# Performance work log

Hardware: AMD Instinct MI355X
Metric: run time of the kernel (lower is better)

## Reference

```python
import jax, jax.numpy as jnp
import numpy as np

B, T, S1, S2 = 8, 64, 128, 128
TD, SD, V, PAD = 512, 512, 32000, 0
EXT = V + S1 + S2
EPS = 1e-5


def _ln(x):
    # F.layer_norm with no affine params (biased variance, eps=1e-5)
    m = x.mean(axis=-1, keepdims=True)
    v = ((x - m) ** 2).mean(axis=-1, keepdims=True)
    return (x - m) / jnp.sqrt(v + EPS)


def _cross_attention(q, k, q_mask, k_mask, attn_w, attn_b, v_vec):
    # attn(cat(q,k)) == q @ Wq^T + k @ Wk^T + b, computed without materializing the concat
    Wq = attn_w[:, :TD]          # [TD, TD] (query part of weight: cat order is (query, key))
    Wk = attn_w[:, TD:]          # [TD, SD]
    sq = jnp.einsum('btd,ed->bte', q, Wq)   # [B,T,TD]
    sk = jnp.einsum('bsd,ed->bse', k, Wk)   # [B,S,TD]
    energy = jnp.tanh(sq[:, :, None, :] + sk[:, None, :, :] + attn_b)  # [B,T,S,TD]
    scores = jnp.einsum('btse,e->bts', energy, v_vec)                  # [B,T,S]
    out_att = scores * k_mask[:, None, :] * q_mask[:, :, None]
    masked = jnp.where((k_mask == PAD)[:, None, :], -jnp.inf, scores)
    attn = jax.nn.softmax(masked, axis=-1)
    weight = jnp.einsum('bts,bsd->btd', attn, k) * q_mask[:, :, None]  # [B,T,SD]
    return out_att, weight


def _scatter_copy(att, map_idx):
    # index_put_(accumulate=True) into [B,T,EXT]
    copy = jnp.zeros((B, T, EXT), dtype=att.dtype)
    b_idx = jnp.arange(B)[:, None, None]
    t_idx = jnp.arange(T)[None, :, None]
    m_idx = map_idx[:, None, :]
    return copy.at[b_idx, t_idx, m_idx].add(att)


def setup_inputs() -> dict:
    key = jax.random.key(0)
    ks = jax.random.split(key, 14)
    sc = 0.02
    return {
        'tgt_dec_out': jax.random.normal(ks[0], (B, T, TD), jnp.float32),
        'src1_key': jax.random.normal(ks[1], (B, S1, SD), jnp.float32),
        'src2_key': jax.random.normal(ks[2], (B, S2, SD), jnp.float32),
        'src1_map_idx': jax.random.randint(ks[3], (B, S1), 0, EXT),
        'src2_map_idx': jax.random.randint(ks[4], (B, S2), 0, EXT),
        'out_fc_w': jax.random.normal(ks[5], (V, TD), jnp.float32) * sc,
        'out_fc_b': jnp.zeros((V,), jnp.float32),
        'attn1_w': jax.random.normal(ks[6], (TD, SD + TD), jnp.float32) * sc,
        'attn1_b': jnp.zeros((TD,), jnp.float32),
        'v1': jax.random.normal(ks[7], (TD,), jnp.float32) * sc,
        'attn2_w': jax.random.normal(ks[8], (TD, SD + TD), jnp.float32) * sc,
        'attn2_b': jnp.zeros((TD,), jnp.float32),
        'v2': jax.random.normal(ks[9], (TD,), jnp.float32) * sc,
        'gate_w': jax.random.normal(ks[10], (3, 2 * SD + TD), jnp.float32) * sc,
        'gate_b': jnp.zeros((3,), jnp.float32),
    }


def reference(tgt_dec_out, src1_key, src2_key, src1_map_idx, src2_map_idx,
              out_fc_w, out_fc_b, attn1_w, attn1_b, v1, attn2_w, attn2_b, v2,
              gate_w, gate_b):
    tgt_output = _ln(jnp.einsum('btd,vd->btv', tgt_dec_out, out_fc_w) + out_fc_b)
    tgt_output = jnp.pad(tgt_output, ((0, 0), (0, 0), (0, S1 + S2)), constant_values=float(PAD))

    tgt_mask = jnp.sign(jnp.abs(tgt_dec_out).sum(-1))   # [B,T]
    src1_mask = jnp.sign(jnp.abs(src1_key).sum(-1))     # [B,S1]
    src2_mask = jnp.sign(jnp.abs(src2_key).sum(-1))     # [B,S2]

    att1, c1 = _cross_attention(tgt_dec_out, src1_key, tgt_mask, src1_mask, attn1_w, attn1_b, v1)
    att1 = _ln(att1)
    copy_output1 = _scatter_copy(att1, src1_map_idx)

    att2, c2 = _cross_attention(tgt_dec_out, src2_key, tgt_mask, src2_mask, attn2_w, attn2_b, v2)
    att2 = _ln(att2)
    copy_output2 = _scatter_copy(att2, src2_map_idx)

    gate_in = jnp.concatenate([tgt_dec_out, c1, c2], axis=-1)  # [B,T,TD+2*SD]
    p = jax.nn.softmax(jnp.einsum('btd,pd->btp', gate_in, gate_w) + gate_b, axis=-1)  # [B,T,3]

    output = (tgt_output * p[..., 0:1]
              + copy_output1 * p[..., 1:2]
              + copy_output2 * p[..., 2:3])
    return output
```

## Files before the change

kernel.cpp:

```cpp
#include <hip/hip_runtime.h>

#define NB 8
#define NT 64
#define NS 128
#define TDIM 512
#define NV 32000
#define NEXT 32256
#define NBT 512
#define LNEPS 1e-5f
#define CLG 2.8853900817779268f

typedef unsigned short u16;
typedef __attribute__((ext_vector_type(8))) short short8;
typedef __attribute__((ext_vector_type(4))) float f32x4;

__device__ __forceinline__ float bf2f(u16 u){ union{unsigned int i; float f;} v; v.i = ((unsigned int)u)<<16; return v.f; }
__device__ __forceinline__ u16 f2bf(float f){ union{float f; unsigned int i;} v; v.f=f; unsigned int r = v.i + 0x7FFFu + ((v.i>>16)&1u); return (u16)(r>>16); }
__device__ __forceinline__ float wsum(float v){
  v += __shfl_xor(v,32); v += __shfl_xor(v,16); v += __shfl_xor(v,8);
  v += __shfl_xor(v,4);  v += __shfl_xor(v,2);  v += __shfl_xor(v,1); return v; }
__device__ __forceinline__ float wmax(float v){
  v = fmaxf(v,__shfl_xor(v,32)); v = fmaxf(v,__shfl_xor(v,16)); v = fmaxf(v,__shfl_xor(v,8));
  v = fmaxf(v,__shfl_xor(v,4));  v = fmaxf(v,__shfl_xor(v,2));  v = fmaxf(v,__shfl_xor(v,1)); return v; }

#define GL2LDS(gp, lp) __builtin_amdgcn_global_load_lds( \
    (__attribute__((address_space(1))) void*)(void*)(gp), \
    (__attribute__((address_space(3))) void*)(void*)(lp), 16, 0, 0)

__global__ __launch_bounds__(256) void k_cast(const float* tgt, const float* s1, const float* s2,
    const float* a1w, const float* a2w, const float* ofw,
    u16* tgtb, u16* s1b, u16* s2b, u16* a1wb, u16* a2wb, u16* ofwb, float* msk)
{
  int blk = blockIdx.x;
  const float* src; u16* dst; int base;
  if(blk < 128){       src=tgt; dst=tgtb;  base=blk; }
  else if(blk < 384){  src=s1;  dst=s1b;   base=blk-128; }
  else if(blk < 640){  src=s2;  dst=s2b;   base=blk-384; }
  else if(blk < 896){  src=a1w; dst=a1wb;  base=blk-640; }
  else if(blk < 1152){ src=a2w; dst=a2wb;  base=blk-896; }
  else {               src=ofw; dst=ofwb;  base=blk-1152; }
  size_t off = (size_t)base*2048 + (size_t)threadIdx.x*8;
  float4 x0 = *(const float4*)(src+off);
  float4 x1 = *(const float4*)(src+off+4);
  float xs[8] = {x0.x,x0.y,x0.z,x0.w,x1.x,x1.y,x1.z,x1.w};
  short8 r;
  #pragma unroll
  for(int j=0;j<8;++j) r[j] = (short)f2bf(xs[j]);
  *(short8*)(dst+off) = r;
  if(blk < 640){
    float a = 0.f;
    #pragma unroll
    for(int j=0;j<8;++j) a += fabsf(xs[j]);
    a = wsum(a);
    if((threadIdx.x&63)==0){
      int w = threadIdx.x>>6;
      int midx;
      if(blk<128)      midx = blk*4 + w;
      else if(blk<384) midx = 512 + (blk-128)*4 + w;
      else             midx = 1536 + (blk-384)*4 + w;
      msk[midx] = (a>0.f) ? 1.f : 0.f;
    }
  }
}

template<int MODE>
__device__ __forceinline__ void gemm_core(const u16* A, int lda, const u16* W, int ldw,
    float* Cf, u16* Cb, int ldc, const float* bias, int K, int bm, int bn, float scale,
    float2* pstats, int nb)
{
  __shared__ u16 Al[128*32];
  __shared__ u16 Wl[128*32];
  __shared__ float ps_s[2][128], pq_s[2][128];
  const int tid = threadIdx.x, lane = tid&63, wv = tid>>6;
  const int wm = wv>>1, wn = wv&1;
  const int fr = lane&15, fq = lane>>4;
  const int lrow = lane>>2;
  const int lcol = (lane&3)*8;
  f32x4 acc[4][4] = {};
  for(int k0=0;k0<K;k0+=32){
    #pragma unroll
    for(int r=0;r<2;++r){
      int c = wv + 4*r;
      int row = c*16 + lrow;
      const u16* ga = A + (size_t)(bm+row)*lda + k0 + lcol;
      const u16* gw = W + (size_t)(bn+row)*ldw + k0 + lcol;
      GL2LDS(ga, &Al[c*512]);
      GL2LDS(gw, &Wl[c*512]);
    }
    __syncthreads();
    short8 af[4], bfr[4];
    #pragma unroll
    for(int m=0;m<4;++m) af[m] = *(const short8*)&Al[(wm*64 + m*16 + fr)*32 + fq*8];
    #pragma unroll
    for(int n=0;n<4;++n) bfr[n] = *(const short8*)&Wl[(wn*64 + n*16 + fr)*32 + fq*8];
    #pragma unroll
    for(int m=0;m<4;++m)
      #pragma unroll
      for(int n=0;n<4;++n)
        acc[m][n] = __builtin_amdgcn_mfma_f32_16x16x32_bf16(af[m], bfr[n], acc[m][n], 0,0,0);
    __syncthreads();
  }
  if(MODE==2){
    #pragma unroll
    for(int m=0;m<4;++m)
      #pragma unroll
      for(int n=0;n<4;++n)
        #pragma unroll
        for(int i=0;i<4;++i){
          int row = bm + wm*64 + m*16 + fq*4 + i;
          int col = bn + wn*64 + n*16 + fr;
          float bv = bias ? bias[col] : 0.f;
          Cf[(size_t)row*ldc + col] = (acc[m][n][i] + bv)*scale;
        }
  } else {
    #pragma unroll
    for(int m=0;m<4;++m){
      float rs_[4]={0,0,0,0}, rq_[4]={0,0,0,0};
      #pragma unroll
      for(int n=0;n<4;++n)
        #pragma unroll
        for(int i=0;i<4;++i){
          int row = bm + wm*64 + m*16 + fq*4 + i;
          int col = bn + wn*64 + n*16 + fr;
          float v = acc[m][n][i] + bias[col];
          Cb[(size_t)row*ldc + col] = f2bf(v);
          rs_[i] += v; rq_[i] += v*v;
        }
      #pragma unroll
      for(int i=0;i<4;++i){
        float a=rs_[i], q=rq_[i];
        a+=__shfl_xor(a,1); a+=__shfl_xor(a,2); a+=__shfl_xor(a,4); a+=__shfl_xor(a,8);
        q+=__shfl_xor(q,1); q+=__shfl_xor(q,2); q+=__shfl_xor(q,4); q+=__shfl_xor(q,8);
        if(fr==0){ int lr = wm*64 + m*16 + fq*4 + i; ps_s[wn][lr]=a; pq_s[wn][lr]=q; }
      }
    }
    __syncthreads();
    if(tid<128){
      float2 pv;
      pv.x = ps_s[0][tid]+ps_s[1][tid];
      pv.y = pq_s[0][tid]+pq_s[1][tid];
      pstats[(size_t)(bm+tid)*250 + nb] = pv;
    }
  }
}

__global__ __launch_bounds__(256) void k_proj(const u16* tgt, const u16* s1, const u16* s2,
    const u16* w1, const u16* w2, const float* b1, const float* b2,
    float* sq1, float* sk1, float* sq2, float* sk2)
{
  int z = blockIdx.z;
  int Mt = (z&1) ? 1024 : 512;
  int bm = blockIdx.y*128; if(bm >= Mt) return;
  const u16* A = (z&1) ? ((z>>1) ? s2 : s1) : tgt;
  const u16* W = ((z>>1) ? w2 : w1) + ((z&1) ? TDIM : 0);
  float* Cf = (z==0) ? sq1 : (z==1) ? sk1 : (z==2) ? sq2 : sk2;
  const float* bias = (z&1) ? nullptr : ((z>>1) ? b2 : b1);
  gemm_core<2>(A, TDIM, W, 2*TDIM, Cf, nullptr, TDIM, bias, TDIM, bm, blockIdx.x*128, CLG, nullptr, 0);
}

__global__ __launch_bounds__(256) void k_big(const u16* tgt, const u16* W, const float* bias,
                                             u16* logits, float2* pstats)
{
  int lid = (blockIdx.x&7)*125 + (blockIdx.x>>3);
  int bm = (lid&3)*128, bn = (lid>>2)*128;
  gemm_core<1>(tgt, TDIM, W, TDIM, nullptr, logits, NV, bias, TDIM, bm, bn, 1.f, pstats, lid>>2);
}

__global__ __launch_bounds__(256) void k_energy(
  const float* sq1, const float* sq2, const float* sk1, const float* sk2,
  const float* v1p, const float* v2p, float* pene)
{
  int lid = (blockIdx.x&7)*128 + (blockIdx.x>>3);
  int src = lid>>9, b = (lid>>6)&7, tc = (lid>>4)&3, sc = (lid>>2)&3, eq = lid&3;
  int tid = threadIdx.x;
  const float* SQ = src? sq2:sq1;
  const float* SK = src? sk2:sk1;
  const float* vp = src? v2p:v1p;
  int t0 = tc*16, s0 = sc*32;
  int strow = tid&31, trow = tid>>5;

  __shared__ float sk_lds[32*65];
  float acc_a = 0.f, acc_b = 0.f;
  const float* sqa = SQ + (size_t)(b*64 + t0 + trow)*512;
  const float* sqb = sqa + 8*512;

  for(int ec=eq*2; ec<eq*2+2; ++ec){
    {
      int r = tid>>3, c0 = (tid&7)*8;
      const float* sp = SK + (size_t)(b*128 + s0 + r)*512 + ec*64 + c0;
      float4 A0 = *(const float4*)sp;
      float4 A1 = *(const float4*)(sp+4);
      float* dp = &sk_lds[r*65 + c0];
      dp[0]=A0.x; dp[1]=A0.y; dp[2]=A0.z; dp[3]=A0.w;
      dp[4]=A1.x; dp[5]=A1.y; dp[6]=A1.z; dp[7]=A1.w;
    }
    __syncthreads();
    #pragma unroll
    for(int sub=0; sub<4; ++sub){
      int e0 = ec*64 + sub*16;
      float4 V0 = *(const float4*)(vp+e0),    V1 = *(const float4*)(vp+e0+4);
      float4 V2 = *(const float4*)(vp+e0+8),  V3 = *(const float4*)(vp+e0+12);
      float4 QA0 = *(const float4*)(sqa+e0),  QA1 = *(const float4*)(sqa+e0+4);
      float4 QA2 = *(const float4*)(sqa+e0+8),QA3 = *(const float4*)(sqa+e0+12);
      float4 QB0 = *(const float4*)(sqb+e0),  QB1 = *(const float4*)(sqb+e0+4);
      float4 QB2 = *(const float4*)(sqb+e0+8),QB3 = *(const float4*)(sqb+e0+12);
      float vv[16] = {V0.x,V0.y,V0.z,V0.w,V1.x,V1.y,V1.z,V1.w,V2.x,V2.y,V2.z,V2.w,V3.x,V3.y,V3.z,V3.w};
      float qa[16] = {QA0.x,QA0.y,QA0.z,QA0.w,QA1.x,QA1.y,QA1.z,QA1.w,QA2.x,QA2.y,QA2.z,QA2.w,QA3.x,QA3.y,QA3.z,QA3.w};
      float qb[16] = {QB0.x,QB0.y,QB0.z,QB0.w,QB1.x,QB1.y,QB1.z,QB1.w,QB2.x,QB2.y,QB2.z,QB2.w,QB3.x,QB3.y,QB3.z,QB3.w};
      const float* skr = &sk_lds[strow*65 + sub*16];
      #pragma unroll
      for(int e=0;e<16;++e){
        float skv = skr[e];
        float ya = qa[e] + skv;
        float yb = qb[e] + skv;
        float ra = __builtin_amdgcn_rcpf(__builtin_amdgcn_exp2f(ya) + 1.f);
        float rb = __builtin_amdgcn_rcpf(__builtin_amdgcn_exp2f(yb) + 1.f);
        acc_a = __builtin_fmaf(vv[e], ra, acc_a);
        acc_b = __builtin_fmaf(vv[e], rb, acc_b);
      }
    }
    __syncthreads();
  }
  size_t ia = (size_t)((eq*2+src)*512 + b*64 + t0 + trow)*128 + s0 + strow;
  pene[ia] = acc_a;
  pene[ia + 8*128] = acc_b;
}

__global__ __launch_bounds__(256) void k_sm(
  const float* pene, const float* v1p, const float* v2p,
  const float* k1g, const float* k2g, const float* msk,
  float* al1, float* al2, float* c1, float* c2)
{
  int lid = (blockIdx.x&7)*32 + (blockIdx.x>>3);
  int src = lid>>7, b = (lid>>4)&7, tq = lid&15;
  int tid = threadIdx.x, lane = tid&63, wv = tid>>6;
  int t = tq*4 + wv, bt = b*64 + t;
  const float* vp = src? v2p:v1p;
  const float* kg = src? k2g:k1g;
  float* al = src? al2:al1;
  float* cc = src? c2:c1;
  const float* km_g = msk + 512 + src*1024 + b*128;
  __shared__ float aw_lds[4][132];
  __shared__ float qm_lds[4];

  {
    float vsp = 0.f;
    #pragma unroll
    for(int r2=0;r2<8;++r2) vsp += vp[lane + 64*r2];
    float Vsum = wsum(vsp);
    float qm = msk[bt];
    float km0 = km_g[lane], km1 = km_g[lane+64];
    size_t pbase = (size_t)(src*512 + bt)*128;
    float p0a = pene[pbase + lane]          + pene[pbase + 131072 + lane];
    float p0b = pene[pbase + 262144 + lane] + pene[pbase + 393216 + lane];
    float p1a = pene[pbase + lane + 64]          + pene[pbase + 131072 + lane + 64];
    float p1b = pene[pbase + 262144 + lane + 64] + pene[pbase + 393216 + lane + 64];
    float s0v = Vsum - 2.f*(p0a + p0b);
    float s1v = Vsum - 2.f*(p1a + p1b);
    float a0 = s0v*km0*qm, a1 = s1v*km1*qm;
    float sm = wsum(a0+a1), sqq = wsum(a0*a0+a1*a1);
    float m0 = km0!=0.f ? s0v : -1e30f;
    float m1 = km1!=0.f ? s1v : -1e30f;
    float mx = wmax(fmaxf(m0,m1));
    float e0 = km0!=0.f ? __expf(s0v-mx) : 0.f;
    float e1 = km1!=0.f ? __expf(s1v-mx) : 0.f;
    float den = wsum(e0+e1);
    float mean = sm/128.f;
    float inv  = rsqrtf(sqq/128.f - mean*mean + LNEPS);
    al[(size_t)bt*128 + lane]      = (a0-mean)*inv;
    al[(size_t)bt*128 + lane + 64] = (a1-mean)*inv;
    float rden = 1.f/den;
    aw_lds[wv][lane]      = e0*rden;
    aw_lds[wv][lane+64]   = e1*rden;
    if(lane==0) qm_lds[wv] = qm;
  }
  __syncthreads();
  {
    float acc[4][2] = {};
    const float* kb = kg + (size_t)b*128*512;
    for(int s=0;s<128;++s){
      float kv0 = kb[(size_t)s*512 + tid];
      float kv1 = kb[(size_t)s*512 + tid + 256];
      #pragma unroll
      for(int w=0;w<4;++w){
        float a = aw_lds[w][s];
        acc[w][0] = __builtin_fmaf(a, kv0, acc[w][0]);
        acc[w][1] = __builtin_fmaf(a, kv1, acc[w][1]);
      }
    }
    #pragma unroll
    for(int w=0;w<4;++w){
      float qm = qm_lds[w];
      size_t o = (size_t)(b*64 + tq*4 + w)*512;
      cc[o + tid]       = qm*acc[w][0];
      cc[o + tid + 256] = qm*acc[w][1];
    }
  }
}

__global__ __launch_bounds__(256) void k_out(const u16* logits, const float2* pstats,
    const float* al1, const float* al2, const float* c1, const float* c2,
    const float* tgt, const float* gw, const float* gb,
    const int* map1, const int* map2, float* out)
{
  int row = blockIdx.x>>2, q = blockIdx.x&3, b = row>>6;
  int tid = threadIdx.x, lane = tid&63, wv = tid>>6;
  __shared__ float gred[4][3], rs[4], rq[4], st[2], pl_s[3];
  __shared__ int hkey[1024];
  __shared__ float hval[1024];
  __shared__ unsigned int bmap[252];

  #pragma unroll
  for(int r=0;r<4;++r){ hkey[tid+256*r] = -1; hval[tid+256*r] = 0.f; }
  if(tid < 252) bmap[tid] = 0u;

  {
    float t0v = tgt[(size_t)row*512+tid], t1v = tgt[(size_t)row*512+tid+256];
    float c10 = c1[(size_t)row*512+tid],  c11 = c1[(size_t)row*512+tid+256];
    float c20 = c2[(size_t)row*512+tid],  c21 = c2[(size_t)row*512+tid+256];
    #pragma unroll
    for(int p=0;p<3;++p){
      const float* gp = gw + p*1536;
      float a = gp[tid]*t0v + gp[tid+256]*t1v
              + gp[512+tid]*c10 + gp[768+tid]*c11
              + gp[1024+tid]*c20 + gp[1280+tid]*c21;
      a = wsum(a);
      if(lane==0) gred[wv][p] = a;
    }
  }
  {
    float s=0.f, qv=0.f;
    if(tid < 250){ float2 pv = pstats[(size_t)row*250 + tid]; s = pv.x; qv = pv.y; }
    s = wsum(s); qv = wsum(qv);
    if(lane==0){ rs[wv]=s; rq[wv]=qv; }
  }
  __syncthreads();
  if(tid==0){
    float S = rs[0]+rs[1]+rs[2]+rs[3];
    float Q = rq[0]+rq[1]+rq[2]+rq[3];
    float mean = S/(float)NV;
    float var  = Q/(float)NV - mean*mean;
    st[0] = mean; st[1] = rsqrtf(var+LNEPS);
    float g0 = gred[0][0]+gred[1][0]+gred[2][0]+gred[3][0] + gb[0];
    float g1 = gred[0][1]+gred[1][1]+gred[2][1]+gred[3][1] + gb[1];
    float g2 = gred[0][2]+gred[1][2]+gred[2][2]+gred[3][2] + gb[2];
    float m = fmaxf(g0, fmaxf(g1, g2));
    float e0=__expf(g0-m), e1=__expf(g1-m), e2=__expf(g2-m);
    float sI = 1.f/(e0+e1+e2);
    pl_s[0]=e0*sI; pl_s[1]=e1*sI; pl_s[2]=e2*sI;
  }
  __syncthreads();

  int elo = q*8064;
  {
    int src = tid>>7, sl = tid&127;
    int e = (src ? map2 : map1)[b*128 + sl];
    if(e >= elo && e < elo+8064){
      float val = pl_s[1+src] * (src ? al2 : al1)[(size_t)row*128 + sl];
      unsigned int h = ((unsigned int)e * 2654435761u) >> 22;
      for(;;){
        int old = atomicCAS(&hkey[h], -1, e);
        if(old == -1 || old == e){ atomicAdd(&hval[h], val); break; }
        h = (h+1) & 1023;
      }
      int rel = e - elo;
      atomicOr(&bmap[rel>>5], 1u << (rel&31));
    }
  }
  __syncthreads();

  float mean = st[0], inv = st[1], p0 = pl_s[0];
  const u16* Lr = logits + (size_t)row*NV;
  float* orow = out + (size_t)row*NEXT;
  for(int i=q*2016+tid; i<(q+1)*2016; i+=256){
    int e0 = i*4;
    float4 r;
    if(e0 < NV){
      const u16* L = &Lr[e0];
      r.x = p0*(bf2f(L[0])-mean)*inv;
      r.y = p0*(bf2f(L[1])-mean)*inv;
      r.z = p0*(bf2f(L[2])-mean)*inv;
      r.w = p0*(bf2f(L[3])-mean)*inv;
    } else { r.x=r.y=r.z=r.w=0.f; }
    int rel = e0 - elo;
    unsigned int w4 = (bmap[rel>>5] >> (rel&31)) & 0xFu;
    if(w4){
      #pragma unroll
      for(int j=0;j<4;++j){
        if(w4 & (1u<<j)){
          int e = e0 + j;
          unsigned int h = ((unsigned int)e * 2654435761u) >> 22;
          while(hkey[h] != e) h = (h+1) & 1023;
          float pv = hval[h];
          if(j==0) r.x += pv; else if(j==1) r.y += pv; else if(j==2) r.z += pv; else r.w += pv;
        }
      }
    }
    *(float4*)&orow[e0] = r;
  }
}

extern "C" void kernel_launch(void* const* d_in, const int* in_sizes, int n_in,
                              void* d_out, int out_size, void* d_ws, size_t ws_size,
                              hipStream_t stream)
{
  const float* tgt  = (const float*)d_in[0];
  const float* s1k  = (const float*)d_in[1];
  const float* s2k  = (const float*)d_in[2];
  const int*   map1 = (const int*)d_in[3];
  const int*   map2 = (const int*)d_in[4];
  const float* ofw  = (const float*)d_in[5];
  const float* ofb  = (const float*)d_in[6];
  const float* a1w  = (const float*)d_in[7];
  const float* a1b  = (const float*)d_in[8];
  const float* v1   = (const float*)d_in[9];
  const float* a2w  = (const float*)d_in[10];
  const float* a2b  = (const float*)d_in[11];
  const float* v2   = (const float*)d_in[12];
  const float* gw   = (const float*)d_in[13];
  const float* gb   = (const float*)d_in[14];

  float* wsf   = (float*)d_ws;
  float* sq1   = wsf;
  float* sq2   = wsf + 262144;
  float* sk1   = wsf + 524288;
  float* sk2   = wsf + 1048576;
  float* al1   = wsf + 1572864;
  float* al2   = wsf + 1638400;
  float* msk   = wsf + 1705984;
  float* c1    = wsf + 1709568;
  float* c2    = wsf + 1971712;
  float* pene  = wsf + 2233856;
  float2* pstats = (float2*)(wsf + 2758144);
  u16*  logits = (u16*)(wsf + 3014144);
  u16*  tgtb   = (u16*)(wsf + 11206144);
  u16*  s1b    = (u16*)(wsf + 11337216);
  u16*  s2b    = (u16*)(wsf + 11599360);
  u16*  a1wb   = (u16*)(wsf + 11861504);
  u16*  a2wb   = (u16*)(wsf + 12123648);
  u16*  ofwb   = (u16*)(wsf + 12385792);
  float* out   = (float*)d_out;

  k_cast   <<<9152, 256, 0, stream>>>(tgt, s1k, s2k, a1w, a2w, ofw, tgtb, s1b, s2b, a1wb, a2wb, ofwb, msk);
  k_proj   <<<dim3(4,8,4), 256, 0, stream>>>(tgtb, s1b, s2b, a1wb, a2wb, a1b, a2b, sq1, sk1, sq2, sk2);
  k_energy <<<1024, 256, 0, stream>>>(sq1, sq2, sk1, sk2, v1, v2, pene);
  k_sm     <<<256, 256, 0, stream>>>(pene, v1, v2, s1k, s2k, msk, al1, al2, c1, c2);
  k_big    <<<1000, 256, 0, stream>>>(tgtb, ofwb, ofb, logits, pstats);
  k_out    <<<2048, 256, 0, stream>>>(logits, pstats, al1, al2, c1, c2, tgt, gw, gb, map1, map2, out);
}
```

Baseline: 121.2 us.

## Rewrite logits GEMM with 256x256 tiles, 512 threads and 4-stage async LDS pipeline

Replaces the shared 128x128 GEMM path for the output-vocab projection with a dedicated kernel using 256x256 tiles, 8 waves, and a 4-buffer LDS ring that keeps two K-steps of global loads in flight via explicit vmcnt waits and raw barriers. It also raises MFMA wave priority and remaps blocks across XCDs, and halves the per-row partial LayerNorm stats to 125 tiles. The goal is to cut global reload traffic and hide load latency behind MFMA work. In exchange the grid drops to 250 blocks, which may underfill the CUs, and LDS use rises sharply.

```diff
diff --git a/kernel.cpp b/kernel.cpp
--- a/kernel.cpp
+++ b/kernel.cpp
@@ -65,12 +65,10 @@
 
 template<int MODE>
 __device__ __forceinline__ void gemm_core(const u16* A, int lda, const u16* W, int ldw,
-    float* Cf, u16* Cb, int ldc, const float* bias, int K, int bm, int bn, float scale,
-    float2* pstats, int nb)
+    float* Cf, int ldc, const float* bias, int K, int bm, int bn, float scale)
 {
   __shared__ u16 Al[128*32];
   __shared__ u16 Wl[128*32];
-  __shared__ float ps_s[2][128], pq_s[2][128];
   const int tid = threadIdx.x, lane = tid&63, wv = tid>>6;
   const int wm = wv>>1, wn = wv&1;
   const int fr = lane&15, fq = lane>>4;
@@ -100,48 +98,17 @@
         acc[m][n] = __builtin_amdgcn_mfma_f32_16x16x32_bf16(af[m], bfr[n], acc[m][n], 0,0,0);
     __syncthreads();
   }
-  if(MODE==2){
-    #pragma unroll
-    for(int m=0;m<4;++m)
-      #pragma unroll
-      for(int n=0;n<4;++n)
-        #pragma unroll
-        for(int i=0;i<4;++i){
-          int row = bm + wm*64 + m*16 + fq*4 + i;
-          int col = bn + wn*64 + n*16 + fr;
-          float bv = bias ? bias[col] : 0.f;
-          Cf[(size_t)row*ldc + col] = (acc[m][n][i] + bv)*scale;
-        }
-  } else {
-    #pragma unroll
-    for(int m=0;m<4;++m){
-      float rs_[4]={0,0,0,0}, rq_[4]={0,0,0,0};
-      #pragma unroll
-      for(int n=0;n<4;++n)
-        #pragma unroll
-        for(int i=0;i<4;++i){
-          int row = bm + wm*64 + m*16 + fq*4 + i;
-          int col = bn + wn*64 + n*16 + fr;
-          float v = acc[m][n][i] + bias[col];
-          Cb[(size_t)row*ldc + col] = f2bf(v);
-          rs_[i] += v; rq_[i] += v*v;
-        }
+  #pragma unroll
+  for(int m=0;m<4;++m)
+    #pragma unroll
+    for(int n=0;n<4;++n)
       #pragma unroll
       for(int i=0;i<4;++i){
-        float a=rs_[i], q=rq_[i];
-        a+=__shfl_xor(a,1); a+=__shfl_xor(a,2); a+=__shfl_xor(a,4); a+=__shfl_xor(a,8);
-        q+=__shfl_xor(q,1); q+=__shfl_xor(q,2); q+=__shfl_xor(q,4); q+=__shfl_xor(q,8);
-        if(fr==0){ int lr = wm*64 + m*16 + fq*4 + i; ps_s[wn][lr]=a; pq_s[wn][lr]=q; }
-      }
-    }
-    __syncthreads();
-    if(tid<128){
-      float2 pv;
-      pv.x = ps_s[0][tid]+ps_s[1][tid];
-      pv.y = pq_s[0][tid]+pq_s[1][tid];
-      pstats[(size_t)(bm+tid)*250 + nb] = pv;
-    }
-  }
+        int row = bm + wm*64 + m*16 + fq*4 + i;
+        int col = bn + wn*64 + n*16 + fr;
+        float bv = bias ? bias[col] : 0.f;
+        Cf[(size_t)row*ldc + col] = (acc[m][n][i] + bv)*scale;
+      }
 }
 
 __global__ __launch_bounds__(256) void k_proj(const u16* tgt, const u16* s1, const u16* s2,
@@ -155,15 +122,93 @@
   const u16* W = ((z>>1) ? w2 : w1) + ((z&1) ? TDIM : 0);
   float* Cf = (z==0) ? sq1 : (z==1) ? sk1 : (z==2) ? sq2 : sk2;
   const float* bias = (z&1) ? nullptr : ((z>>1) ? b2 : b1);
-  gemm_core<2>(A, TDIM, W, 2*TDIM, Cf, nullptr, TDIM, bias, TDIM, bm, blockIdx.x*128, CLG, nullptr, 0);
-}
-
-__global__ __launch_bounds__(256) void k_big(const u16* tgt, const u16* W, const float* bias,
+  gemm_core<2>(A, TDIM, W, 2*TDIM, Cf, TDIM, bias, TDIM, bm, blockIdx.x*128, CLG);
+}
+
+__global__ __launch_bounds__(512) void k_big(const u16* A, const u16* W, const float* bias,
                                              u16* logits, float2* pstats)
 {
-  int lid = (blockIdx.x&7)*125 + (blockIdx.x>>3);
-  int bm = (lid&3)*128, bn = (lid>>2)*128;
-  gemm_core<1>(tgt, TDIM, W, TDIM, nullptr, logits, NV, bias, TDIM, bm, bn, 1.f, pstats, lid>>2);
+  int orig = blockIdx.x;
+  int xcd = orig & 7, idx = orig >> 3;
+  const int q = 31, r = 2;
+  int lid = (xcd < r ? xcd*(q+1) : r*(q+1) + (xcd-r)*q) + idx;
+  int bm = (lid & 1) * 256;
+  int bn = (lid >> 1) * 256;
+
+  __shared__ u16 Asl[4][8192];
+  __shared__ u16 Bsl[4][8192];
+  __shared__ float ps_s[4][256], pq_s[4][256];
+
+  const int tid = threadIdx.x, lane = tid & 63, wv = tid >> 6;
+  const int wm = wv >> 2, wn = wv & 3;
+  const int fr = lane & 15, fq = lane >> 4;
+
+  const u16* Ag0 = A + (size_t)(bm + (tid>>2))*512 + (tid&3)*8;
+  const u16* Wg0 = W + (size_t)(bn + (tid>>2))*512 + (tid&3)*8;
+  u16* Ad0 = &Asl[0][(size_t)(wv*64)*8];
+  u16* Bd0 = &Bsl[0][(size_t)(wv*64)*8];
+
+  #define STAGE(T) { int _s = (T)&3; const u16* _a = Ag0 + (T)*32; const u16* _w = Wg0 + (T)*32; \
+    u16* _ad = Ad0 + (size_t)_s*8192; u16* _bd = Bd0 + (size_t)_s*8192; \
+    GL2LDS(_a, _ad); GL2LDS(_a + 128*512, _ad + 4096); \
+    GL2LDS(_w, _bd); GL2LDS(_w + 128*512, _bd + 4096); }
+
+  f32x4 acc[8][4] = {};
+
+  STAGE(0); STAGE(1);
+  asm volatile("s_waitcnt vmcnt(4)" ::: "memory");
+  __builtin_amdgcn_s_barrier();
+
+  for(int T=0; T<16; ++T){
+    if(T+2 < 16) STAGE(T+2);
+    const u16* As = Asl[T&3];
+    const u16* Bs = Bsl[T&3];
+    short8 af[8], bf[4];
+    #pragma unroll
+    for(int m=0;m<8;++m) af[m] = *(const short8*)&As[(wm*128 + m*16 + fr)*32 + fq*8];
+    #pragma unroll
+    for(int n=0;n<4;++n) bf[n] = *(const short8*)&Bs[(wn*64 + n*16 + fr)*32 + fq*8];
+    __builtin_amdgcn_s_setprio(1);
+    #pragma unroll
+    for(int m=0;m<8;++m)
+      #pragma unroll
+      for(int n=0;n<4;++n)
+        acc[m][n] = __builtin_amdgcn_mfma_f32_16x16x32_bf16(af[m], bf[n], acc[m][n], 0,0,0);
+    __builtin_amdgcn_s_setprio(0);
+    if(T < 14)      { asm volatile("s_waitcnt vmcnt(4)" ::: "memory"); }
+    else if(T == 14){ asm volatile("s_waitcnt vmcnt(0)" ::: "memory"); }
+    if(T < 15) __builtin_amdgcn_s_barrier();
+  }
+
+  #pragma unroll
+  for(int m=0;m<8;++m){
+    float rs_[4]={0,0,0,0}, rq_[4]={0,0,0,0};
+    #pragma unroll
+    for(int n=0;n<4;++n)
+      #pragma unroll
+      for(int i=0;i<4;++i){
+        int row = bm + wm*128 + m*16 + fq*4 + i;
+        int col = bn + wn*64 + n*16 + fr;
+        float v = acc[m][n][i] + bias[col];
+        logits[(size_t)row*NV + col] = f2bf(v);
+        rs_[i] += v; rq_[i] += v*v;
+      }
+    #pragma unroll
+    for(int i=0;i<4;++i){
+      float a=rs_[i], qv=rq_[i];
+      a+=__shfl_xor(a,1); a+=__shfl_xor(a,2); a+=__shfl_xor(a,4); a+=__shfl_xor(a,8);
+      qv+=__shfl_xor(qv,1); qv+=__shfl_xor(qv,2); qv+=__shfl_xor(qv,4); qv+=__shfl_xor(qv,8);
+      if(fr==0){ int lr = wm*128 + m*16 + fq*4 + i; ps_s[wn][lr]=a; pq_s[wn][lr]=qv; }
+    }
+  }
+  __syncthreads();
+  if(tid < 256){
+    float2 pv;
+    pv.x = ps_s[0][tid]+ps_s[1][tid]+ps_s[2][tid]+ps_s[3][tid];
+    pv.y = pq_s[0][tid]+pq_s[1][tid]+pq_s[2][tid]+pq_s[3][tid];
+    pstats[(size_t)(bm+tid)*125 + (bn>>8)] = pv;
+  }
+  #undef STAGE
 }
 
 __global__ __launch_bounds__(256) void k_energy(
@@ -330,7 +375,7 @@
   }
   {
     float s=0.f, qv=0.f;
-    if(tid < 250){ float2 pv = pstats[(size_t)row*250 + tid]; s = pv.x; qv = pv.y; }
+    if(tid < 125){ float2 pv = pstats[(size_t)row*125 + tid]; s = pv.x; qv = pv.y; }
     s = wsum(s); qv = wsum(qv);
     if(lane==0){ rs[wv]=s; rq[wv]=qv; }
   }
@@ -445,6 +490,6 @@
   k_proj   <<<dim3(4,8,4), 256, 0, stream>>>(tgtb, s1b, s2b, a1wb, a2wb, a1b, a2b, sq1, sk1, sq2, sk2);
   k_energy <<<1024, 256, 0, stream>>>(sq1, sq2, sk1, sk2, v1, v2, pene);
   k_sm     <<<256, 256, 0, stream>>>(pene, v1, v2, s1k, s2k, msk, al1, al2, c1, c2);
-  k_big    <<<1000, 256, 0, stream>>>(tgtb, ofwb, ofb, logits, pstats);
+  k_big    <<<250, 512, 0, stream>>>(tgtb, ofwb, ofb, logits, pstats);
   k_out    <<<2048, 256, 0, stream>>>(logits, pstats, al1, al2, c1, c2, tgt, gw, gb, map1, map2, out);
 }
```

New measurement: 121.4 us. No clear change (+0.2%).
